# Optimization experiments

Hardware: AMD Instinct MI355X
Metric: run time of the kernel (lower is better)

## Reference

```python
import jax, jax.numpy as jnp
import numpy as np

EPS = 1e-5  # BatchNorm eps (torch default); BN is in training mode with gamma=1, beta=0 (init values)


def bn(x, axes):
    m = jnp.mean(x, axis=axes, keepdims=True)
    v = jnp.var(x, axis=axes, keepdims=True)
    return (x - m) * jax.lax.rsqrt(v + EPS)


def knn_idx(xyz, k):
    # brute-force squared-distance matrix [B,N,N], k smallest
    d = jnp.sum((xyz[:, :, None, :] - xyz[:, None, :, :]) ** 2, axis=-1)
    _, idx = jax.lax.top_k(-d, k)
    return idx  # [B,N,k]


def gather(x, idx):
    # x: [B,N,C], idx: [B,N,k] -> [B,N,k,C]
    return jax.vmap(lambda a, i: a[i])(x, idx)


def lse(xyz, features, idx, w):
    nbr_xyz = gather(xyz, idx)                       # [B,N,k,3]
    rel = nbr_xyz - xyz[:, :, None, :]
    dist = jnp.sqrt(jnp.maximum(jnp.sum(rel ** 2, -1, keepdims=True), 1e-12))
    nbr_f = gather(features, idx)                    # [B,N,k,C]
    enc = jnp.concatenate([rel, dist, nbr_f], -1)    # [B,N,k,C+4]
    return jax.nn.relu(bn(jnp.einsum('bnkc,oc->bnko', enc, w), (0, 1, 2)))


def att_pool(x, sw1, sw2, sb2, mw):
    # x: [B,N,k,C]
    h = jax.nn.relu(bn(jnp.einsum('bnkc,oc->bnko', x, sw1), (0, 1, 2)))
    scores = jax.nn.softmax(jnp.einsum('bnkc,oc->bnko', h, sw2) + sb2, axis=2)  # softmax over k
    feat = jnp.sum(x * scores, axis=2)               # [B,N,C]
    return jax.nn.relu(bn(jnp.einsum('bnc,oc->bno', feat, mw), (0, 1)))


def drb(x, w1, w2):
    # in_channels == out_channels -> identity shortcut
    h = jax.nn.relu(bn(jnp.einsum('bnc,oc->bno', x, w1), (0, 1)))
    h = bn(jnp.einsum('bnc,oc->bno', h, w2), (0, 1))
    return jax.nn.relu(h + x)


def setup_inputs() -> dict:
    key = jax.random.key(0)
    B, N, C, K, OUT = 4, 8192, 32, 16, 128
    H = OUT // 2  # 64
    ks = jax.random.split(key, 16)
    s = 0.05
    return {
        'xyz': jax.random.normal(ks[0], (B, N, 3), jnp.float32),
        'features': jax.random.normal(ks[1], (B, N, C), jnp.float32),
        'w_lse1': jax.random.normal(ks[2], (H, C + 4), jnp.float32) * s,
        'w_lse2': jax.random.normal(ks[3], (H, C + 4), jnp.float32) * s,
        'ap1_sw1': jax.random.normal(ks[4], (H, H), jnp.float32) * s,
        'ap1_sw2': jax.random.normal(ks[5], (1, H), jnp.float32) * s,
        'ap1_sb2': jax.random.normal(ks[6], (1,), jnp.float32) * s,
        'ap1_mw': jax.random.normal(ks[7], (H, H), jnp.float32) * s,
        'ap2_sw1': jax.random.normal(ks[8], (H, H), jnp.float32) * s,
        'ap2_sw2': jax.random.normal(ks[9], (1, H), jnp.float32) * s,
        'ap2_sb2': jax.random.normal(ks[10], (1,), jnp.float32) * s,
        'ap2_mw': jax.random.normal(ks[11], (H, H), jnp.float32) * s,
        'drb_w1': jax.random.normal(ks[12], (OUT, OUT), jnp.float32) * s,
        'drb_w2': jax.random.normal(ks[13], (OUT, OUT), jnp.float32) * s,
    }


def reference(xyz, features, w_lse1, w_lse2, ap1_sw1, ap1_sw2, ap1_sb2, ap1_mw,
              ap2_sw1, ap2_sw2, ap2_sb2, ap2_mw, drb_w1, drb_w2):
    K = 16
    idx = knn_idx(xyz, K)  # original calls knn twice on same xyz -> identical indices
    f1 = att_pool(lse(xyz, features, idx, w_lse1), ap1_sw1, ap1_sw2, ap1_sb2, ap1_mw)
    f2 = att_pool(lse(xyz, features, idx, w_lse2), ap2_sw1, ap2_sw2, ap2_sb2, ap2_mw)
    agg = jnp.concatenate([f1, f2], axis=-1)  # [B,N,128]
    return drb(agg, drb_w1, drb_w2)           # [B,N,128]
```

## Files before the change

kernel.cpp:

```cpp
#include <hip/hip_runtime.h>
#include <hip/hip_bf16.h>
#include <hip/hip_fp16.h>
#include <float.h>
#include <math.h>

#define DEVFN __device__ __forceinline__

DEVFN void wavefence() { __builtin_amdgcn_wave_barrier(); }

using half8 = __attribute__((ext_vector_type(8))) _Float16;
using f32x4 = __attribute__((ext_vector_type(4))) float;

namespace {
constexpr int Bq = 4, Nq = 8192, Cq = 32, Kq = 16;
constexpr int PTS = Bq * Nq;
constexpr int CH = 16;
constexpr int CAND = Nq / CH;
constexpr double ROWS = 524288.0;

constexpr int DS_Y = 0, DS_Z = 256, DS_G = 512, DS_H1 = 768, DS_H2 = 1024;

constexpr size_t OFF_KD   = 0;
constexpr size_t OFF_KJ   = (size_t)32 << 20;
constexpr size_t OFF_X0   = 0;
constexpr size_t OFF_X1   = (size_t)64 << 20;
constexpr size_t OFF_H1   = 0;
constexpr size_t OFF_H2   = (size_t)16 << 20;
constexpr size_t OFF_GRAW = (size_t)192 << 20;
constexpr size_t OFF_AGG  = (size_t)208 << 20;
constexpr size_t OFF_IDX  = (size_t)224 << 20;
constexpr size_t OFF_DST  = (size_t)226 << 20;
constexpr size_t OFF_MST  = ((size_t)226 << 20) + 10240;
constexpr size_t OFF_BNP  = ((size_t)226 << 20) + 16384;
constexpr size_t WS_NEED  = ((size_t)226 << 20) + 32768;
constexpr size_t FB_GRAW  = (size_t)64 << 20;
constexpr size_t FB_AGG   = (size_t)80 << 20;
constexpr size_t FB_H1    = (size_t)96 << 20;
constexpr size_t FB_H2    = (size_t)112 << 20;
constexpr size_t FB_IDX   = (size_t)128 << 20;
constexpr size_t FB_DST   = (size_t)130 << 20;
constexpr size_t FB_MST   = ((size_t)130 << 20) + 10240;
constexpr size_t FB_BNP   = ((size_t)130 << 20) + 16384;
}

DEVFN void ce_asc(float& a, float& b) {
  const float lo = fminf(a, b), hi = fmaxf(a, b);
  a = lo; b = hi;
}

DEVFN void topk16_update(float* __restrict__ L, float* __restrict__ d) {
#pragma unroll
  for (int k = 2; k <= 16; k <<= 1) {
#pragma unroll
    for (int j = k >> 1; j > 0; j >>= 1) {
#pragma unroll
      for (int i = 0; i < 16; ++i) {
        const int l = i ^ j;
        if (l > i) {
          if ((i & k) == 0) {
            const float lo = fminf(d[i], d[l]), hi = fmaxf(d[i], d[l]);
            d[i] = lo; d[l] = hi;
          } else {
            const float lo = fminf(d[i], d[l]), hi = fmaxf(d[i], d[l]);
            d[i] = hi; d[l] = lo;
          }
        }
      }
    }
  }
#pragma unroll
  for (int i = 0; i < 16; ++i) L[i] = fminf(L[i], d[15 - i]);
#pragma unroll
  for (int j = 8; j > 0; j >>= 1) {
#pragma unroll
    for (int i = 0; i < 16; ++i) {
      const int l = i ^ j;
      if (l > i) ce_asc(L[i], L[l]);
    }
  }
}

DEVFN float distf(const float4 c, const float qx, const float qy, const float qz) {
  const float dx = qx - c.x, dy = qy - c.y, dz = qz - c.z;
  return __fadd_rn(__fadd_rn(__fmul_rn(dx, dx), __fmul_rn(dy, dy)), __fmul_rn(dz, dz));
}

__global__ __launch_bounds__(256, 4) void knn_chunk_kernel(const float* __restrict__ xyz,
                                                           float* __restrict__ pd,
                                                           int* __restrict__ pj) {
  const int b = blockIdx.z;
  const int ch = blockIdx.y;
  const int n = blockIdx.x * 256 + threadIdx.x;
  __shared__ __align__(16) float4 tile[CAND];
  const float* xb = xyz + (size_t)b * Nq * 3;
  for (int t = threadIdx.x; t < CAND; t += 256) {
    const int j = ch * CAND + t;
    tile[t] = make_float4(xb[j * 3], xb[j * 3 + 1], xb[j * 3 + 2], 0.f);
  }
  __syncthreads();
  const float qx = xb[n * 3], qy = xb[n * 3 + 1], qz = xb[n * 3 + 2];
  float L[16];
#pragma unroll
  for (int i = 0; i < 16; ++i) L[i] = FLT_MAX;
  for (int t = 0; t < CAND; t += 16) {
    float d[16];
#pragma unroll
    for (int u = 0; u < 16; ++u) d[u] = distf(tile[t + u], qx, qy, qz);
    topk16_update(L, d);
  }
  const float kth = L[15];
  const size_t base = (((size_t)b * Nq + n) * CH + ch) * Kq;
  int cnt = 0, tfirst = -1;
  for (int t = 0; t < CAND; ++t) {
    const float d = distf(tile[t], qx, qy, qz);
    if (d < kth) { pd[base + cnt] = d; pj[base + cnt] = ch * CAND + t; ++cnt; }
    tfirst = (d == kth && tfirst < 0) ? t : tfirst;
  }
  if (cnt == 15) {
    pd[base + 15] = kth; pj[base + 15] = ch * CAND + tfirst; cnt = 16;
  }
  if (__any(cnt < 16)) {
    for (int t = 0; t < CAND; ++t) {
      const float d = distf(tile[t], qx, qy, qz);
      if (d == kth && cnt < 16) { pd[base + cnt] = d; pj[base + cnt] = ch * CAND + t; ++cnt; }
    }
  }
}

__global__ __launch_bounds__(256, 4) void knn_merge_kernel(const float* __restrict__ pd,
                                                           const int* __restrict__ pj,
                                                           int* __restrict__ idxo) {
  const int q = blockIdx.x * 256 + threadIdx.x;
  const float* dp = pd + (size_t)q * CH * Kq;
  const int* jp = pj + (size_t)q * CH * Kq;
  float L[16];
#pragma unroll
  for (int i = 0; i < 16; ++i) L[i] = FLT_MAX;
  for (int t = 0; t < CH * Kq; t += 16) {
    float d[16];
#pragma unroll
    for (int u = 0; u < 16; u += 4) {
      const float4 v = *(const float4*)(dp + t + u);
      d[u] = v.x; d[u + 1] = v.y; d[u + 2] = v.z; d[u + 3] = v.w;
    }
    topk16_update(L, d);
  }
  const float kth = L[15];
  int* op = idxo + (size_t)q * Kq;
  int cnt = 0;
  for (int t = 0; t < CH * Kq; ++t) {
    const float d = dp[t];
    if (d < kth) { op[cnt] = jp[t]; ++cnt; }
  }
  for (int t = 0; t < CH * Kq; ++t) {
    const float d = dp[t];
    if (d == kth && cnt < 16) { op[cnt] = jp[t]; ++cnt; }
  }
}

struct PF { float4 f0, f1; float nx, ny, nz; };

DEVFN PF issue_feat(const float* __restrict__ features, const float* __restrict__ xyz,
                    int p, int j, int sub) {
  const int b = p >> 13;
  const float* fr = features + ((size_t)b * Nq + j) * Cq;
  const float* xb = xyz + ((size_t)b * Nq + j) * 3;
  PF r;
  r.f0 = *(const float4*)(fr + sub * 8);
  r.f1 = *(const float4*)(fr + sub * 8 + 4);
  r.nx = xb[0]; r.ny = xb[1]; r.nz = xb[2];
  return r;
}

DEVFN int issue_idx(const int* __restrict__ idx, int p, int lane) {
  return idx[(size_t)p * Kq + (lane >> 2)];
}

DEVFN float3 issue_query(const float* __restrict__ xyz, int p) {
  const float* q = xyz + (size_t)p * 3;
  return make_float3(q[0], q[1], q[2]);
}

DEVFN void commit_enc(__half* __restrict__ enc, int lane, const PF& pf,
                      float qx, float qy, float qz) {
  const int k = lane >> 2, sub = lane & 3;
  __half* er = enc + k * 40;
  union { float4 f; __half2 h[4]; } u;
  u.h[0] = __floats2half2_rn(pf.f0.x, pf.f0.y);
  u.h[1] = __floats2half2_rn(pf.f0.z, pf.f0.w);
  u.h[2] = __floats2half2_rn(pf.f1.x, pf.f1.y);
  u.h[3] = __floats2half2_rn(pf.f1.z, pf.f1.w);
  *(float4*)(er + sub * 8) = u.f;
  if (sub == 0) {
    const float rx = pf.nx - qx, ry = pf.ny - qy, rz = pf.nz - qz;
    const float ss = rx * rx + ry * ry + rz * rz;
    const float dd = sqrtf(fmaxf(ss, 1e-12f));
    __half2* rd = (__half2*)(er + 32);
    rd[0] = __floats2half2_rn(rx, ry);
    rd[1] = __floats2half2_rn(rz, dd);
  }
}

DEVFN void commit_enc128(__half* __restrict__ enc, int lane, const PF& pf,
                         float qx, float qy, float qz) {
  const int k = lane >> 2, sub = lane & 3;
  char* base = (char*)enc + k * 128;
  union { float4 f; __half2 h[4]; } u;
  u.h[0] = __floats2half2_rn(pf.f0.x, pf.f0.y);
  u.h[1] = __floats2half2_rn(pf.f0.z, pf.f0.w);
  u.h[2] = __floats2half2_rn(pf.f1.x, pf.f1.y);
  u.h[3] = __floats2half2_rn(pf.f1.z, pf.f1.w);
  *(float4*)(base + ((sub ^ (k & 7)) * 16)) = u.f;
  if (sub == 0) {
    const float rx = pf.nx - qx, ry = pf.ny - qy, rz = pf.nz - qz;
    const float ss = rx * rx + ry * ry + rz * rz;
    const float dd = sqrtf(fmaxf(ss, 1e-12f));
    __half2* aux = (__half2*)(base + ((4 ^ (k & 7)) * 16));
    aux[0] = __floats2half2_rn(rx, ry);
    aux[1] = __floats2half2_rn(rz, dd);
  }
}

DEVFN void zero_enc_pad(__half* __restrict__ enc, int lane) {
  if (lane < 16) {
    const __half2 z2 = __floats2half2_rn(0.f, 0.f);
    __half2* pz = (__half2*)(enc + lane * 40 + 36);
    pz[0] = z2; pz[1] = z2;
  }
}

DEVFN float dot40h(const __half* __restrict__ er, const __half2* __restrict__ wh2) {
  float a0 = 0.f, a1 = 0.f, a2 = 0.f, a3 = 0.f;
#pragma unroll
  for (int r = 0; r < 5; ++r) {
    union { float4 f; __half2 h[4]; } u;
    u.f = *(const float4*)(er + r * 8);
#pragma unroll
    for (int q = 0; q < 4; ++q) {
      const __half2 xv = u.h[q];
      const __half2 wv = wh2[r * 4 + q];
      if (q & 1) {
        a2 += __low2float(xv) * __low2float(wv);
        a3 += __high2float(xv) * __high2float(wv);
      } else {
        a0 += __low2float(xv) * __low2float(wv);
        a1 += __high2float(xv) * __high2float(wv);
      }
    }
  }
  return (a0 + a1) + (a2 + a3);
}

DEVFN float dot64x(const __half* __restrict__ xr, const __half2* __restrict__ sh2) {
  float a0 = 0.f, a1 = 0.f, a2 = 0.f, a3 = 0.f;
#pragma unroll
  for (int r = 0; r < 8; ++r) {
    union { float4 f; __half2 h[4]; } u;
    u.f = *(const float4*)(xr + r * 8);
#pragma unroll
    for (int q = 0; q < 4; ++q) {
      const __half2 xv = u.h[q];
      const __half2 wv = sh2[r * 4 + q];
      if (q & 1) {
        a2 += __low2float(xv) * __low2float(wv);
        a3 += __high2float(xv) * __high2float(wv);
      } else {
        a0 += __low2float(xv) * __low2float(wv);
        a1 += __high2float(xv) * __high2float(wv);
      }
    }
  }
  return (a0 + a1) + (a2 + a3);
}

DEVFN void load_w40(const float* __restrict__ Wrow, __half2* wh2) {
#pragma unroll
  for (int c = 0; c < 16; ++c)
    wh2[c] = __floats2half2_rn(Wrow[4 + 2 * c], Wrow[5 + 2 * c]);
  wh2[16] = __floats2half2_rn(Wrow[0], Wrow[1]);
  wh2[17] = __floats2half2_rn(Wrow[2], Wrow[3]);
  wh2[18] = __floats2half2_rn(0.f, 0.f);
  wh2[19] = wh2[18];
}

DEVFN void load_b1(const float* __restrict__ W, int lane, half8* b1) {
  const int o16 = lane & 15, q = lane >> 4;
#pragma unroll
  for (int t = 0; t < 4; ++t) {
    const int o = t * 16 + o16;
#pragma unroll
    for (int ks = 0; ks < 2; ++ks) {
      half8 v;
#pragma unroll
      for (int j = 0; j < 8; ++j) {
        const int s = ks * 32 + q * 8 + j;
        float wv = 0.f;
        if (s < 36) { const int orig = (s < 32) ? (s + 4) : (s - 32); wv = W[o * 36 + orig]; }
        v[j] = (_Float16)wv;
      }
      b1[t * 2 + ks] = v;
    }
  }
}

DEVFN void load_b2(const float* __restrict__ S1, int lane, half8* b2) {
  const int o16 = lane & 15, q = lane >> 4;
#pragma unroll
  for (int t = 0; t < 4; ++t) {
    const int o = t * 16 + o16;
#pragma unroll
    for (int ks = 0; ks < 2; ++ks) {
      half8 v;
#pragma unroll
      for (int j = 0; j < 8; ++j) {
        const int c = ks * 32 + q * 8 + j;
        v[j] = (_Float16)S1[o * 64 + c];
      }
      b2[t * 2 + ks] = v;
    }
  }
}

#define GATHER_PROLOGUE                                                      \
  int p = wid;                                                               \
  int jc = issue_idx(idx, p, lane);                                          \
  PF cur = issue_feat(features, xyz, p, jc, lane & 3);                       \
  float3 qc = issue_query(xyz, p);                                           \
  int pn0 = p + nw; if (pn0 >= PTS) pn0 = p;                                 \
  int jn = issue_idx(idx, pn0, lane);                                        \
  float3 qn = issue_query(xyz, pn0);                                         \
  for (; p < PTS; p += nw) {                                                 \
    int pn = p + nw; if (pn >= PTS) pn = p;                                  \
    int pn2 = pn + nw; if (pn2 >= PTS) pn2 = pn;                             \
    PF nxt = issue_feat(features, xyz, pn, jn, lane & 3);                    \
    const int jn2 = issue_idx(idx, pn2, lane);                               \
    const float3 q2 = issue_query(xyz, pn2);                                 \
    commit_enc(enc, lane, cur, qc.x, qc.y, qc.z);                            \
    wavefence();

#define GATHER_PROLOGUE_M                                                    \
  int p = wid;                                                               \
  int jc = issue_idx(idx, p, lane);                                          \
  PF cur = issue_feat(features, xyz, p, jc, lane & 3);                       \
  float3 qc = issue_query(xyz, p);                                           \
  int pn0 = p + nw; if (pn0 >= PTS) pn0 = p;                                 \
  int jn = issue_idx(idx, pn0, lane);                                        \
  float3 qn = issue_query(xyz, pn0);                                         \
  for (; p < PTS; p += nw) {                                                 \
    int pn = p + nw; if (pn >= PTS) pn = p;                                  \
    int pn2 = pn + nw; if (pn2 >= PTS) pn2 = pn;                             \
    PF nxt = issue_feat(features, xyz, pn, jn, lane & 3);                    \
    const int jn2 = issue_idx(idx, pn2, lane);                               \
    const float3 q2 = issue_query(xyz, pn2);                                 \
    commit_enc128(enc, lane, cur, qc.x, qc.y, qc.z);                         \
    wavefence();

#define GATHER_EPILOGUE                                                      \
    wavefence();                                                             \
    cur = nxt; qc = qn; qn = q2; jn = jn2;                                   \
  }

__global__ __launch_bounds__(256) void encM_kernel(const float* __restrict__ xyz,
                                                   const float* __restrict__ features,
                                                   const int* __restrict__ idx,
                                                   float* __restrict__ mstat) {
  __shared__ __align__(16) __half encS[4][16 * 40];
  __shared__ float mred[4][36 * 37];
  const int lane = threadIdx.x & 63, wv = threadIdx.x >> 6;
  __half* enc = encS[wv];
  zero_enc_pad(enc, lane);
  wavefence();
  const int li = (lane < 36) ? lane : 0;
  float macc[36];
#pragma unroll
  for (int i = 0; i < 36; ++i) macc[i] = 0.f;
  float vacc = 0.f;
  const int wid = blockIdx.x * 4 + wv, nw = gridDim.x * 4;
  GATHER_PROLOGUE
#pragma unroll
    for (int k = 0; k < 16; ++k) {
      const __half* er = enc + k * 40;
      const float ei = __half2float(er[li]);
      vacc += ei;
#pragma unroll
      for (int r = 0; r < 5; ++r) {
        union { float4 f; __half2 h[4]; } u;
        u.f = *(const float4*)(er + r * 8);
#pragma unroll
        for (int q = 0; q < 4; ++q) {
          const int s = r * 8 + 2 * q;
          if (s < 36)     macc[s]     += ei * __low2float(u.h[q]);
          if (s + 1 < 36) macc[s + 1] += ei * __high2float(u.h[q]);
        }
      }
    }
  GATHER_EPILOGUE
  if (lane < 36) {
#pragma unroll
    for (int j = 0; j < 36; ++j) mred[wv][lane * 37 + j] = macc[j];
    mred[wv][lane * 37 + 36] = vacc;
  }
  __syncthreads();
  for (int t = threadIdx.x; t < 36 * 37; t += 256) {
    const float s = mred[0][t] + mred[1][t] + mred[2][t] + mred[3][t];
    atomicAdd(&mstat[t], s);
  }
}

__global__ void y_finalize_kernel(const float* __restrict__ mstat,
                                  const float* __restrict__ wl1,
                                  const float* __restrict__ wl2,
                                  float* __restrict__ bnp) {
  const int t = threadIdx.x;
  const int br = t >> 6, o = t & 63;
  const float* W = br ? wl2 : wl1;
  double wrow[36];
  for (int s = 0; s < 36; ++s) {
    const int orig = (s < 32) ? (s + 4) : (s - 32);
    wrow[s] = (double)W[o * 36 + orig];
  }
  double mean = 0.0, ey2 = 0.0;
  for (int i = 0; i < 36; ++i) {
    mean += wrow[i] * (double)mstat[i * 37 + 36];
    double rowacc = 0.0;
    for (int j = 0; j < 36; ++j) rowacc += wrow[j] * (double)mstat[i * 37 + j];
    ey2 += wrow[i] * rowacc;
  }
  const double invR = 1.0 / ROWS;
  mean *= invR; ey2 *= invR;
  const double var = ey2 - mean * mean;
  bnp[DS_Y + br * 64 + o] = (float)mean;
  bnp[DS_Y + 128 + br * 64 + o] = (float)(1.0 / sqrt(var + 1e-5));
}

__global__ void bn_finalize_kernel(const double* __restrict__ dstat, float* __restrict__ bnp,
                                   int base, double invc) {
  const int t = threadIdx.x;
  const double m = dstat[base + t] * invc;
  const double v = dstat[base + 128 + t] * invc - m * m;
  bnp[base + t] = (float)m;
  bnp[base + 128 + t] = (float)(1.0 / sqrt(v + 1e-5));
}

__global__ __launch_bounds__(256)
void passA2_mat_kernel(const float* __restrict__ xyz,
                       const float* __restrict__ features,
                       const int* __restrict__ idx,
                       const float* __restrict__ wl1,
                       const float* __restrict__ wl2,
                       const float* __restrict__ bnp,
                       __half* __restrict__ x0buf,
                       __half* __restrict__ x1buf) {
  __shared__ __align__(16) __half encS[4][16 * 64];
  __shared__ __align__(16) __half xS[4][16 * 64];
  const int lane = threadIdx.x & 63, wv = threadIdx.x >> 6;
  __half* enc = encS[wv];
  __half* xL = xS[wv];
  {
    const float4 z4 = {0.f, 0.f, 0.f, 0.f};
    ((float4*)enc)[lane] = z4;
    ((float4*)enc)[lane + 64] = z4;
  }
  wavefence();
  half8 b1a[8], b1b[8];
  load_b1(wl1, lane, b1a);
  load_b1(wl2, lane, b1b);
  const int r16 = lane & 15, q4 = lane >> 4;
  float ym0[4], ys0[4], ym1[4], ys1[4];
#pragma unroll
  for (int t = 0; t < 4; ++t) {
    ym0[t] = bnp[DS_Y + t * 16 + r16];
    ys0[t] = bnp[DS_Y + 128 + t * 16 + r16];
    ym1[t] = bnp[DS_Y + 64 + t * 16 + r16];
    ys1[t] = bnp[DS_Y + 128 + 64 + t * 16 + r16];
  }
  const int wid = blockIdx.x * 4 + wv, nw = gridDim.x * 4;
  GATHER_PROLOGUE_M
    const char* encb = (const char*)enc + r16 * 128;
    const half8 a0 = *(const half8*)(encb + (((q4)     ^ (r16 & 7)) * 16));
    const half8 a1 = *(const half8*)(encb + (((4 + q4) ^ (r16 & 7)) * 16));
    {
      f32x4 yt[4];
#pragma unroll
      for (int t = 0; t < 4; ++t) {
        f32x4 acc = {0.f, 0.f, 0.f, 0.f};
        acc = __builtin_amdgcn_mfma_f32_16x16x32_f16(a0, b1a[t * 2], acc, 0, 0, 0);
        acc = __builtin_amdgcn_mfma_f32_16x16x32_f16(a1, b1a[t * 2 + 1], acc, 0, 0, 0);
        yt[t] = acc;
      }
#pragma unroll
      for (int t = 0; t < 4; ++t) {
        const int col = t * 16 + r16;
        const int chk = col >> 3;
#pragma unroll
        for (int rr = 0; rr < 4; ++rr) {
          const int row = q4 * 4 + rr;
          float xv = (yt[t][rr] - ym0[t]) * ys0[t];
          xv = xv > 0.f ? xv : 0.f;
          *(_Float16*)((char*)xL + row * 128 + ((chk ^ (row & 7)) * 16) + (col & 7) * 2) =
              (_Float16)xv;
        }
      }
      wavefence();
#pragma unroll
      for (int it = 0; it < 2; ++it) {
        const int chunk = it * 64 + lane;
        const int row = chunk >> 3, c8 = chunk & 7;
        const float4 xv4 = *(const float4*)((const char*)xL + row * 128 + ((c8 ^ (row & 7)) * 16));
        *(float4*)((char*)x0buf + (size_t)p * 2048 + chunk * 16) = xv4;
      }
      wavefence();
    }
    {
      f32x4 yt[4];
#pragma unroll
      for (int t = 0; t < 4; ++t) {
        f32x4 acc = {0.f, 0.f, 0.f, 0.f};
        acc = __builtin_amdgcn_mfma_f32_16x16x32_f16(a0, b1b[t * 2], acc, 0, 0, 0);
        acc = __builtin_amdgcn_mfma_f32_16x16x32_f16(a1, b1b[t * 2 + 1], acc, 0, 0, 0);
        yt[t] = acc;
      }
#pragma unroll
      for (int t = 0; t < 4; ++t) {
        const int col = t * 16 + r16;
        const int chk = col >> 3;
#pragma unroll
        for (int rr = 0; rr < 4; ++rr) {
          const int row = q4 * 4 + rr;
          float xv = (yt[t][rr] - ym1[t]) * ys1[t];
          xv = xv > 0.f ? xv : 0.f;
          *(_Float16*)((char*)xL + row * 128 + ((chk ^ (row & 7)) * 16) + (col & 7) * 2) =
              (_Float16)xv;
        }
      }
      wavefence();
#pragma unroll
      for (int it = 0; it < 2; ++it) {
        const int chunk = it * 64 + lane;
        const int row = chunk >> 3, c8 = chunk & 7;
        const float4 xv4 = *(const float4*)((const char*)xL + row * 128 + ((c8 ^ (row & 7)) * 16));
        *(float4*)((char*)x1buf + (size_t)p * 2048 + chunk * 16) = xv4;
      }
    }
  GATHER_EPILOGUE
}

__global__ __launch_bounds__(256)
void zstat_kernel(const __half* __restrict__ x0, const __half* __restrict__ x1,
                  const float* __restrict__ s1a, const float* __restrict__ s1b,
                  double* __restrict__ dstat) {
  const int lane = threadIdx.x & 63, wv = threadIdx.x >> 6;
  half8 b2a[8], b2b[8];
  load_b2(s1a, lane, b2a);
  load_b2(s1b, lane, b2b);
  const int r16 = lane & 15, q4 = lane >> 4;
  float sa1[4] = {0.f, 0.f, 0.f, 0.f}, sa2[4] = {0.f, 0.f, 0.f, 0.f};
  float sb1[4] = {0.f, 0.f, 0.f, 0.f}, sb2s[4] = {0.f, 0.f, 0.f, 0.f};
  const int wid = blockIdx.x * 4 + wv, nw = gridDim.x * 4;
  for (int p = wid; p < PTS; p += nw) {
    const size_t abase = (size_t)p * 1024 + r16 * 64 + q4 * 8;
    const half8 xa0 = *(const half8*)(x0 + abase);
    const half8 xa1 = *(const half8*)(x0 + abase + 32);
    const half8 xb0 = *(const half8*)(x1 + abase);
    const half8 xb1 = *(const half8*)(x1 + abase + 32);
#pragma unroll
    for (int t = 0; t < 4; ++t) {
      f32x4 acc = {0.f, 0.f, 0.f, 0.f};
      acc = __builtin_amdgcn_mfma_f32_16x16x32_f16(xa0, b2a[t * 2], acc, 0, 0, 0);
      acc = __builtin_amdgcn_mfma_f32_16x16x32_f16(xa1, b2a[t * 2 + 1], acc, 0, 0, 0);
#pragma unroll
      for (int rr = 0; rr < 4; ++rr) { const float zv = acc[rr]; sa1[t] += zv; sa2[t] += zv * zv; }
      f32x4 acc2 = {0.f, 0.f, 0.f, 0.f};
      acc2 = __builtin_amdgcn_mfma_f32_16x16x32_f16(xb0, b2b[t * 2], acc2, 0, 0, 0);
      acc2 = __builtin_amdgcn_mfma_f32_16x16x32_f16(xb1, b2b[t * 2 + 1], acc2, 0, 0, 0);
#pragma unroll
      for (int rr = 0; rr < 4; ++rr) { const float zv = acc2[rr]; sb1[t] += zv; sb2s[t] += zv * zv; }
    }
  }
#pragma unroll
  for (int t = 0; t < 4; ++t) {
    sa1[t] += __shfl_xor(sa1[t], 16, 64);  sa1[t] += __shfl_xor(sa1[t], 32, 64);
    sa2[t] += __shfl_xor(sa2[t], 16, 64);  sa2[t] += __shfl_xor(sa2[t], 32, 64);
    sb1[t] += __shfl_xor(sb1[t], 16, 64);  sb1[t] += __shfl_xor(sb1[t], 32, 64);
    sb2s[t] += __shfl_xor(sb2s[t], 16, 64); sb2s[t] += __shfl_xor(sb2s[t], 32, 64);
  }
  if (lane < 16) {
#pragma unroll
    for (int t = 0; t < 4; ++t) {
      atomicAdd(&dstat[DS_Z + t * 16 + lane], (double)sa1[t]);
      atomicAdd(&dstat[DS_Z + 128 + t * 16 + lane], (double)sa2[t]);
      atomicAdd(&dstat[DS_Z + 64 + t * 16 + lane], (double)sb1[t]);
      atomicAdd(&dstat[DS_Z + 128 + 64 + t * 16 + lane], (double)sb2s[t]);
    }
  }
}

__global__ __launch_bounds__(256)
void passB2_mat_kernel(const __half* __restrict__ xbuf,
                       const float* __restrict__ S1,
                       const float* __restrict__ s2,
                       const float* __restrict__ sb,
                       const float* __restrict__ mw,
                       const float* __restrict__ bnp,
                       double* __restrict__ dstat,
                       float* __restrict__ graw,
                       int br) {
  __shared__ __align__(16) __half2 mwl2[64 * 34];
  __shared__ __align__(16) float featL[4][64];
  __shared__ __align__(16) float zS[4][16 * 64];
  for (int t = threadIdx.x; t < 64 * 32; t += 256) {
    const int r = t >> 5, c2 = t & 31;
    mwl2[r * 34 + c2] = __floats2half2_rn(mw[r * 64 + c2 * 2], mw[r * 64 + c2 * 2 + 1]);
  }
  __syncthreads();
  const int lane = threadIdx.x & 63, wv = threadIdx.x >> 6;
  const int r16 = lane & 15, q4 = lane >> 4;
  half8 b2[8];
  load_b2(S1, lane, b2);
  const __half2* mrow = mwl2 + lane * 34;
  const float zm = bnp[DS_Z + br * 64 + lane];
  const float zsc = bnp[DS_Z + 128 + br * 64 + lane];
  const float sw2r = s2[lane];
  const float sb2v = sb[0];
  float gs1 = 0.f, gs2 = 0.f;
  float* zw = &zS[wv][0];
  const int wid = blockIdx.x * 4 + wv, nw = gridDim.x * 4;
  for (int p = wid; p < PTS; p += nw) {
    const size_t abase = (size_t)p * 1024 + r16 * 64 + q4 * 8;
    const half8 xa0 = *(const half8*)(xbuf + abase);
    const half8 xa1 = *(const half8*)(xbuf + abase + 32);
#pragma unroll
    for (int t = 0; t < 4; ++t) {
      f32x4 acc = {0.f, 0.f, 0.f, 0.f};
      acc = __builtin_amdgcn_mfma_f32_16x16x32_f16(xa0, b2[t * 2], acc, 0, 0, 0);
      acc = __builtin_amdgcn_mfma_f32_16x16x32_f16(xa1, b2[t * 2 + 1], acc, 0, 0, 0);
#pragma unroll
      for (int rr = 0; rr < 4; ++rr)
        zw[(q4 * 4 + rr) * 64 + t * 16 + r16] = acc[rr];
    }
    wavefence();
    const __half* xr = xbuf + (size_t)p * 1024 + lane;
    const float* zr = zw + lane;
    float xv[16], pl[16];
#pragma unroll
    for (int k = 0; k < 16; ++k) {
      xv[k] = __half2float(xr[k * 64]);
      float h = (zr[k * 64] - zm) * zsc;
      h = h > 0.f ? h : 0.f;
      pl[k] = h * sw2r;
    }
#pragma unroll
    for (int off = 1; off < 64; off <<= 1) {
#pragma unroll
      for (int k = 0; k < 16; ++k) pl[k] += __shfl_xor(pl[k], off, 64);
    }
    float mx = -FLT_MAX;
#pragma unroll
    for (int k = 0; k < 16; ++k) { pl[k] += sb2v; mx = fmaxf(mx, pl[k]); }
    float se = 0.f;
#pragma unroll
    for (int k = 0; k < 16; ++k) { pl[k] = expf(pl[k] - mx); se += pl[k]; }
    const float inv = 1.f / se;
    float f = 0.f;
#pragma unroll
    for (int k = 0; k < 16; ++k) f += xv[k] * (pl[k] * inv);
    featL[wv][lane] = f;
    wavefence();
    const float* featW = &featL[wv][0];
    float g0 = 0.f, g1 = 0.f, g2 = 0.f, g3 = 0.f;
#pragma unroll
    for (int c8 = 0; c8 < 8; ++c8) {
      const float4 fa = *(const float4*)(featW + c8 * 8);
      const float4 fb = *(const float4*)(featW + c8 * 8 + 4);
      const __half2 m0 = mrow[c8 * 4 + 0];
      const __half2 m1 = mrow[c8 * 4 + 1];
      const __half2 m2 = mrow[c8 * 4 + 2];
      const __half2 m3 = mrow[c8 * 4 + 3];
      g0 += fa.x * __low2float(m0); g1 += fa.y * __high2float(m0);
      g2 += fa.z * __low2float(m1); g3 += fa.w * __high2float(m1);
      g0 += fb.x * __low2float(m2); g1 += fb.y * __high2float(m2);
      g2 += fb.z * __low2float(m3); g3 += fb.w * __high2float(m3);
    }
    const float g = (g0 + g1) + (g2 + g3);
    graw[((size_t)br * PTS + p) * 64 + lane] = g;
    gs1 += g; gs2 += g * g;
    wavefence();
  }
  atomicAdd(&dstat[DS_G + br * 64 + lane], (double)gs1);
  atomicAdd(&dstat[DS_G + 128 + br * 64 + lane], (double)gs2);
}

__global__ __launch_bounds__(256)
void passA_kernel(const float* __restrict__ xyz,
                  const float* __restrict__ features,
                  const int* __restrict__ idx,
                  const float* __restrict__ wl1,
                  const float* __restrict__ wl2,
                  const float* __restrict__ s1a,
                  const float* __restrict__ s1b,
                  const float* __restrict__ bnp,
                  double* __restrict__ dstat) {
  const int br = blockIdx.y;
  const float* W = br ? wl2 : wl1;
  const float* S1 = br ? s1b : s1a;
  __shared__ __align__(16) __half encS[4][16 * 40];
  __shared__ __align__(16) __half xS[4][16 * 64];
  const int lane = threadIdx.x & 63, wv = threadIdx.x >> 6;
  __half* enc = encS[wv];
  __half* xL = xS[wv];
  zero_enc_pad(enc, lane);
  wavefence();
  __half2 wh2[20];
  load_w40(W + lane * 36, wh2);
  __half2 sh2[32];
#pragma unroll
  for (int c = 0; c < 32; ++c)
    sh2[c] = __floats2half2_rn(S1[lane * 64 + 2 * c], S1[lane * 64 + 2 * c + 1]);
  const float ym = bnp[DS_Y + br * 64 + lane];
  const float ys = bnp[DS_Y + 128 + br * 64 + lane];
  float zs1 = 0.f, zs2 = 0.f;
  const int wid = blockIdx.x * 4 + wv, nw = gridDim.x * 4;
  GATHER_PROLOGUE
#pragma unroll
    for (int k = 0; k < 16; ++k) {
      float xv = (dot40h(enc + k * 40, wh2) - ym) * ys;
      xv = xv > 0.f ? xv : 0.f;
      xL[k * 64 + lane] = __float2half(xv);
    }
    wavefence();
#pragma unroll
    for (int k = 0; k < 16; ++k) {
      const float acc = dot64x(xL + k * 64, sh2);
      zs1 += acc; zs2 += acc * acc;
    }
  GATHER_EPILOGUE
  atomicAdd(&dstat[DS_Z + br * 64 + lane], (double)zs1);
  atomicAdd(&dstat[DS_Z + 128 + br * 64 + lane], (double)zs2);
}

__global__ __launch_bounds__(256)
void passB_kernel(const float* __restrict__ xyz,
                  const float* __restrict__ features,
                  const int* __restrict__ idx,
                  const float* __restrict__ wl1,
                  const float* __restrict__ wl2,
                  const float* __restrict__ s1a,
                  const float* __restrict__ s1b,
                  const float* __restrict__ s2a,
                  const float* __restrict__ s2b,
                  const float* __restrict__ sba,
                  const float* __restrict__ sbb,
                  const float* __restrict__ mwa,
                  const float* __restrict__ mwb,
                  const float* __restrict__ bnp,
                  double* __restrict__ dstat,
                  float* __restrict__ graw) {
  const int br = blockIdx.y;
  const float* W = br ? wl2 : wl1;
  const float* S1 = br ? s1b : s1a;
  const float* S2 = br ? s2b : s2a;
  const float* SB = br ? sbb : sba;
  const float* MW = br ? mwb : mwa;
  __shared__ __align__(16) __half2 mwl2[64 * 34];
  __shared__ __align__(16) __half encS[4][16 * 40];
  __shared__ __align__(16) __half xS[4][16 * 64];
  __shared__ __align__(16) float featL[4][64];
  for (int t = threadIdx.x; t < 64 * 32; t += 256) {
    const int r = t >> 5, c2 = t & 31;
    mwl2[r * 34 + c2] = __floats2half2_rn(MW[r * 64 + c2 * 2], MW[r * 64 + c2 * 2 + 1]);
  }
  __syncthreads();
  const int lane = threadIdx.x & 63, wv = threadIdx.x >> 6;
  __half* enc = encS[wv];
  __half* xL = xS[wv];
  zero_enc_pad(enc, lane);
  wavefence();
  const __half2* mrow = mwl2 + lane * 34;
  __half2 wh2[20];
  load_w40(W + lane * 36, wh2);
  __half2 sh2[32];
#pragma unroll
  for (int c = 0; c < 32; ++c)
    sh2[c] = __floats2half2_rn(S1[lane * 64 + 2 * c], S1[lane * 64 + 2 * c + 1]);
  const float ym = bnp[DS_Y + br * 64 + lane];
  const float ys = bnp[DS_Y + 128 + br * 64 + lane];
  const float zm = bnp[DS_Z + br * 64 + lane];
  const float zs = bnp[DS_Z + 128 + br * 64 + lane];
  const float sw2r = S2[lane];
  const float sb2v = SB[0];
  float gs1 = 0.f, gs2 = 0.f;
  const int wid = blockIdx.x * 4 + wv, nw = gridDim.x * 4;
  GATHER_PROLOGUE
#pragma unroll
    for (int k = 0; k < 16; ++k) {
      float xv = (dot40h(enc + k * 40, wh2) - ym) * ys;
      xv = xv > 0.f ? xv : 0.f;
      xL[k * 64 + lane] = __float2half(xv);
    }
    wavefence();
    float pl[16];
#pragma unroll
    for (int k = 0; k < 16; ++k) {
      float h = (dot64x(xL + k * 64, sh2) - zm) * zs;
      h = h > 0.f ? h : 0.f;
      pl[k] = h * sw2r;
    }
#pragma unroll
    for (int off = 1; off < 64; off <<= 1) {
#pragma unroll
      for (int k = 0; k < 16; ++k) pl[k] += __shfl_xor(pl[k], off, 64);
    }
    float mx = -FLT_MAX;
#pragma unroll
    for (int k = 0; k < 16; ++k) { pl[k] += sb2v; mx = fmaxf(mx, pl[k]); }
    float se = 0.f;
#pragma unroll
    for (int k = 0; k < 16; ++k) { pl[k] = expf(pl[k] - mx); se += pl[k]; }
    const float inv = 1.f / se;
    float f = 0.f;
#pragma unroll
    for (int k = 0; k < 16; ++k) f += __half2float(xL[k * 64 + lane]) * (pl[k] * inv);
    featL[wv][lane] = f;
    wavefence();
    const float* featW = &featL[wv][0];
    float g0 = 0.f, g1 = 0.f, g2 = 0.f, g3 = 0.f;
#pragma unroll
    for (int c8 = 0; c8 < 8; ++c8) {
      const float4 fa = *(const float4*)(featW + c8 * 8);
      const float4 fb = *(const float4*)(featW + c8 * 8 + 4);
      const __half2 m0 = mrow[c8 * 4 + 0];
      const __half2 m1 = mrow[c8 * 4 + 1];
      const __half2 m2 = mrow[c8 * 4 + 2];
      const __half2 m3 = mrow[c8 * 4 + 3];
      g0 += fa.x * __low2float(m0); g1 += fa.y * __high2float(m0);
      g2 += fa.z * __low2float(m1); g3 += fa.w * __high2float(m1);
      g0 += fb.x * __low2float(m2); g1 += fb.y * __high2float(m2);
      g2 += fb.z * __low2float(m3); g3 += fb.w * __high2float(m3);
    }
    const float g = (g0 + g1) + (g2 + g3);
    graw[((size_t)br * PTS + p) * 64 + lane] = g;
    gs1 += g; gs2 += g * g;
  GATHER_EPILOGUE
  atomicAdd(&dstat[DS_G + br * 64 + lane], (double)gs1);
  atomicAdd(&dstat[DS_G + 128 + br * 64 + lane], (double)gs2);
}

__global__ __launch_bounds__(256) void drb_mm_kernel(const float* __restrict__ in,
                                                     const float* __restrict__ wmat,
                                                     const float* __restrict__ bnp,
                                                     double* __restrict__ dstat,
                                                     float* __restrict__ aggout,
                                                     float* __restrict__ rowout,
                                                     int bpIn, int dsOut, int mode) {
  __shared__ __align__(16) float wlds[128 * 129];
  __shared__ __align__(16) float rowS[4][128];
  for (int t = threadIdx.x; t < 128 * 128; t += 256) wlds[(t >> 7) * 129 + (t & 127)] = wmat[t];
  __syncthreads();
  const int lane = threadIdx.x & 63, wv = threadIdx.x >> 6;
  const float m0 = bnp[bpIn + lane], s0 = bnp[bpIn + 128 + lane];
  const float m1 = bnp[bpIn + 64 + lane], s1 = bnp[bpIn + 128 + 64 + lane];
  float a1s0 = 0.f, a1s1 = 0.f, a2s0 = 0.f, a2s1 = 0.f;
  const int wid = blockIdx.x * 4 + wv, nw = gridDim.x * 4;
  for (int p = wid; p < PTS; p += nw) {
    float v0, v1;
    if (mode == 0) {
      v0 = in[(size_t)p * 64 + lane];
      v1 = in[(size_t)PTS * 64 + (size_t)p * 64 + lane];
    } else {
      v0 = in[(size_t)p * 128 + lane];
      v1 = in[(size_t)p * 128 + 64 + lane];
    }
    v0 = (v0 - m0) * s0; v0 = v0 > 0.f ? v0 : 0.f;
    v1 = (v1 - m1) * s1; v1 = v1 > 0.f ? v1 : 0.f;
    rowS[wv][lane] = v0;
    rowS[wv][64 + lane] = v1;
    if (aggout) {
      aggout[(size_t)p * 128 + lane] = v0;
      aggout[(size_t)p * 128 + 64 + lane] = v1;
    }
    wavefence();
#pragma unroll
    for (int h = 0; h < 2; ++h) {
      const int o = h * 64 + lane;
      float b0 = 0.f, b1 = 0.f, b2 = 0.f, b3 = 0.f;
#pragma unroll
      for (int c4 = 0; c4 < 32; ++c4) {
        const float4 rv = *(const float4*)(&rowS[wv][c4 * 4]);
        b0 += rv.x * wlds[o * 129 + c4 * 4 + 0];
        b1 += rv.y * wlds[o * 129 + c4 * 4 + 1];
        b2 += rv.z * wlds[o * 129 + c4 * 4 + 2];
        b3 += rv.w * wlds[o * 129 + c4 * 4 + 3];
      }
      const float acc = (b0 + b1) + (b2 + b3);
      rowout[(size_t)p * 128 + o] = acc;
      if (h == 0) { a1s0 += acc; a2s0 += acc * acc; }
      else        { a1s1 += acc; a2s1 += acc * acc; }
    }
    wavefence();
  }
  atomicAdd(&dstat[dsOut + lane], (double)a1s0);
  atomicAdd(&dstat[dsOut + 64 + lane], (double)a1s1);
  atomicAdd(&dstat[dsOut + 128 + lane], (double)a2s0);
  atomicAdd(&dstat[dsOut + 128 + 64 + lane], (double)a2s1);
}

__global__ __launch_bounds__(256) void final_kernel(const float* __restrict__ h2,
                                                    const float* __restrict__ agg,
                                                    const float* __restrict__ bnp,
                                                    float* __restrict__ out) {
  const size_t e = (size_t)blockIdx.x * 256 + threadIdx.x;
  const int ch = (int)(e & 127);
  const float m = bnp[DS_H2 + ch], s = bnp[DS_H2 + 128 + ch];
  float v = (h2[e] - m) * s + agg[e];
  out[e] = v > 0.f ? v : 0.f;
}

extern "C" void kernel_launch(void* const* d_in, const int* in_sizes, int n_in,
                              void* d_out, int out_size, void* d_ws, size_t ws_size,
                              hipStream_t stream) {
  (void)in_sizes; (void)n_in; (void)out_size;
  const float* xyz      = (const float*)d_in[0];
  const float* features = (const float*)d_in[1];
  const float* w_lse1   = (const float*)d_in[2];
  const float* w_lse2   = (const float*)d_in[3];
  const float* ap1_sw1  = (const float*)d_in[4];
  const float* ap1_sw2  = (const float*)d_in[5];
  const float* ap1_sb2  = (const float*)d_in[6];
  const float* ap1_mw   = (const float*)d_in[7];
  const float* ap2_sw1  = (const float*)d_in[8];
  const float* ap2_sw2  = (const float*)d_in[9];
  const float* ap2_sb2  = (const float*)d_in[10];
  const float* ap2_mw   = (const float*)d_in[11];
  const float* drb_w1   = (const float*)d_in[12];
  const float* drb_w2   = (const float*)d_in[13];

  char* ws = (char*)d_ws;
  const bool mat = (ws_size >= WS_NEED);

  float*  knn_d = (float*)(ws + OFF_KD);
  int*    knn_j = (int*)(ws + OFF_KJ);
  int*    idx   = (int*)(ws + (mat ? OFF_IDX : FB_IDX));
  double* dstat = (double*)(ws + (mat ? OFF_DST : FB_DST));
  float*  mstat = (float*)(ws + (mat ? OFF_MST : FB_MST));
  float*  bnp   = (float*)(ws + (mat ? OFF_BNP : FB_BNP));
  float*  graw  = (float*)(ws + (mat ? OFF_GRAW : FB_GRAW));
  float*  agg   = (float*)(ws + (mat ? OFF_AGG : FB_AGG));
  float*  h1    = (float*)(ws + (mat ? OFF_H1 : FB_H1));
  float*  h2    = (float*)(ws + (mat ? OFF_H2 : FB_H2));
  float*  out   = (float*)d_out;

  (void)hipMemsetAsync(dstat, 0, 1280 * sizeof(double) + 36 * 37 * sizeof(float), stream);

  knn_chunk_kernel<<<dim3(Nq / 256, CH, Bq), 256, 0, stream>>>(xyz, knn_d, knn_j);
  knn_merge_kernel<<<dim3(PTS / 256), 256, 0, stream>>>(knn_d, knn_j, idx);

  encM_kernel<<<dim3(1280), 256, 0, stream>>>(xyz, features, idx, mstat);
  y_finalize_kernel<<<1, 128, 0, stream>>>(mstat, w_lse1, w_lse2, bnp);

  if (mat) {
    __half* x0 = (__half*)(ws + OFF_X0);
    __half* x1 = (__half*)(ws + OFF_X1);
    passA2_mat_kernel<<<dim3(1280), 256, 0, stream>>>(xyz, features, idx, w_lse1, w_lse2,
                                                      bnp, x0, x1);
    zstat_kernel<<<dim3(1024), 256, 0, stream>>>(x0, x1, ap1_sw1, ap2_sw1, dstat);
    bn_finalize_kernel<<<1, 128, 0, stream>>>(dstat, bnp, DS_Z, 1.0 / ROWS);
    passB2_mat_kernel<<<dim3(1024), 256, 0, stream>>>(x0, ap1_sw1, ap1_sw2, ap1_sb2,
                                                      ap1_mw, bnp, dstat, graw, 0);
    passB2_mat_kernel<<<dim3(1024), 256, 0, stream>>>(x1, ap2_sw1, ap2_sw2, ap2_sb2,
                                                      ap2_mw, bnp, dstat, graw, 1);
  } else {
    passA_kernel<<<dim3(640, 2), 256, 0, stream>>>(xyz, features, idx, w_lse1, w_lse2,
                                                   ap1_sw1, ap2_sw1, bnp, dstat);
    bn_finalize_kernel<<<1, 128, 0, stream>>>(dstat, bnp, DS_Z, 1.0 / ROWS);
    passB_kernel<<<dim3(512, 2), 256, 0, stream>>>(xyz, features, idx, w_lse1, w_lse2,
                                                   ap1_sw1, ap2_sw1, ap1_sw2, ap2_sw2,
                                                   ap1_sb2, ap2_sb2, ap1_mw, ap2_mw,
                                                   bnp, dstat, graw);
  }
  bn_finalize_kernel<<<1, 128, 0, stream>>>(dstat, bnp, DS_G, 1.0 / PTS);

  drb_mm_kernel<<<dim3(512), 256, 0, stream>>>(graw, drb_w1, bnp, dstat, agg, h1,
                                               DS_G, DS_H1, 0);
  bn_finalize_kernel<<<1, 128, 0, stream>>>(dstat, bnp, DS_H1, 1.0 / PTS);

  drb_mm_kernel<<<dim3(512), 256, 0, stream>>>(h1, drb_w2, bnp, dstat, nullptr, h2,
                                               DS_H1, DS_H2, 1);
  bn_finalize_kernel<<<1, 128, 0, stream>>>(dstat, bnp, DS_H2, 1.0 / PTS);

  final_kernel<<<dim3(PTS * 128 / 256), 256, 0, stream>>>(h2, agg, bnp, out);
}
```

Measured before the change: 1.259 ms.

## Materialize fp16 neighbor encodings in encM and stream them in passA2

The moment-statistics kernel now writes each point's 16x40 fp16 neighbor encoding to a workspace buffer. The second pass reads that buffer with contiguous loads instead of redoing the random neighbor gathers from xyz/features and rebuilding the swizzled LDS encoding. This trades repeated scattered gathers and the extra LDS staging for about 40 MB of extra global writes and reads. The grid size of the second pass also changes.

```diff
diff --git a/kernel.cpp b/kernel.cpp
--- a/kernel.cpp
+++ b/kernel.cpp
@@ -24,6 +24,7 @@
 constexpr size_t OFF_KJ   = (size_t)32 << 20;
 constexpr size_t OFF_X0   = 0;
 constexpr size_t OFF_X1   = (size_t)64 << 20;
+constexpr size_t OFF_ENC  = (size_t)128 << 20;
 constexpr size_t OFF_H1   = 0;
 constexpr size_t OFF_H2   = (size_t)16 << 20;
 constexpr size_t OFF_GRAW = (size_t)192 << 20;
@@ -201,26 +202,6 @@
   }
 }
 
-DEVFN void commit_enc128(__half* __restrict__ enc, int lane, const PF& pf,
-                         float qx, float qy, float qz) {
-  const int k = lane >> 2, sub = lane & 3;
-  char* base = (char*)enc + k * 128;
-  union { float4 f; __half2 h[4]; } u;
-  u.h[0] = __floats2half2_rn(pf.f0.x, pf.f0.y);
-  u.h[1] = __floats2half2_rn(pf.f0.z, pf.f0.w);
-  u.h[2] = __floats2half2_rn(pf.f1.x, pf.f1.y);
-  u.h[3] = __floats2half2_rn(pf.f1.z, pf.f1.w);
-  *(float4*)(base + ((sub ^ (k & 7)) * 16)) = u.f;
-  if (sub == 0) {
-    const float rx = pf.nx - qx, ry = pf.ny - qy, rz = pf.nz - qz;
-    const float ss = rx * rx + ry * ry + rz * rz;
-    const float dd = sqrtf(fmaxf(ss, 1e-12f));
-    __half2* aux = (__half2*)(base + ((4 ^ (k & 7)) * 16));
-    aux[0] = __floats2half2_rn(rx, ry);
-    aux[1] = __floats2half2_rn(rz, dd);
-  }
-}
-
 DEVFN void zero_enc_pad(__half* __restrict__ enc, int lane) {
   if (lane < 16) {
     const __half2 z2 = __floats2half2_rn(0.f, 0.f);
@@ -338,23 +319,6 @@
     commit_enc(enc, lane, cur, qc.x, qc.y, qc.z);                            \
     wavefence();
 
-#define GATHER_PROLOGUE_M                                                    \
-  int p = wid;                                                               \
-  int jc = issue_idx(idx, p, lane);                                          \
-  PF cur = issue_feat(features, xyz, p, jc, lane & 3);                       \
-  float3 qc = issue_query(xyz, p);                                           \
-  int pn0 = p + nw; if (pn0 >= PTS) pn0 = p;                                 \
-  int jn = issue_idx(idx, pn0, lane);                                        \
-  float3 qn = issue_query(xyz, pn0);                                         \
-  for (; p < PTS; p += nw) {                                                 \
-    int pn = p + nw; if (pn >= PTS) pn = p;                                  \
-    int pn2 = pn + nw; if (pn2 >= PTS) pn2 = pn;                             \
-    PF nxt = issue_feat(features, xyz, pn, jn, lane & 3);                    \
-    const int jn2 = issue_idx(idx, pn2, lane);                               \
-    const float3 q2 = issue_query(xyz, pn2);                                 \
-    commit_enc128(enc, lane, cur, qc.x, qc.y, qc.z);                         \
-    wavefence();
-
 #define GATHER_EPILOGUE                                                      \
     wavefence();                                                             \
     cur = nxt; qc = qn; qn = q2; jn = jn2;                                   \
@@ -363,7 +327,8 @@
 __global__ __launch_bounds__(256) void encM_kernel(const float* __restrict__ xyz,
                                                    const float* __restrict__ features,
                                                    const int* __restrict__ idx,
-                                                   float* __restrict__ mstat) {
+                                                   float* __restrict__ mstat,
+                                                   __half* __restrict__ encb) {
   __shared__ __align__(16) __half encS[4][16 * 40];
   __shared__ float mred[4][36 * 37];
   const int lane = threadIdx.x & 63, wv = threadIdx.x >> 6;
@@ -391,6 +356,16 @@
           const int s = r * 8 + 2 * q;
           if (s < 36)     macc[s]     += ei * __low2float(u.h[q]);
           if (s + 1 < 36) macc[s + 1] += ei * __high2float(u.h[q]);
+        }
+      }
+    }
+    if (encb) {
+#pragma unroll
+      for (int it = 0; it < 2; ++it) {
+        const int c = it * 64 + lane;
+        if (c < 80) {
+          const float4 v = *(const float4*)((const char*)enc + c * 16);
+          *(float4*)((char*)encb + (size_t)p * 1280 + c * 16) = v;
         }
       }
     }
@@ -443,25 +418,15 @@
 }
 
 __global__ __launch_bounds__(256)
-void passA2_mat_kernel(const float* __restrict__ xyz,
-                       const float* __restrict__ features,
-                       const int* __restrict__ idx,
-                       const float* __restrict__ wl1,
-                       const float* __restrict__ wl2,
-                       const float* __restrict__ bnp,
-                       __half* __restrict__ x0buf,
-                       __half* __restrict__ x1buf) {
-  __shared__ __align__(16) __half encS[4][16 * 64];
+void passA2s_kernel(const __half* __restrict__ encbuf,
+                    const float* __restrict__ wl1,
+                    const float* __restrict__ wl2,
+                    const float* __restrict__ bnp,
+                    __half* __restrict__ x0buf,
+                    __half* __restrict__ x1buf) {
   __shared__ __align__(16) __half xS[4][16 * 64];
   const int lane = threadIdx.x & 63, wv = threadIdx.x >> 6;
-  __half* enc = encS[wv];
   __half* xL = xS[wv];
-  {
-    const float4 z4 = {0.f, 0.f, 0.f, 0.f};
-    ((float4*)enc)[lane] = z4;
-    ((float4*)enc)[lane + 64] = z4;
-  }
-  wavefence();
   half8 b1a[8], b1b[8];
   load_b1(wl1, lane, b1a);
   load_b1(wl2, lane, b1b);
@@ -475,10 +440,13 @@
     ys1[t] = bnp[DS_Y + 128 + 64 + t * 16 + r16];
   }
   const int wid = blockIdx.x * 4 + wv, nw = gridDim.x * 4;
-  GATHER_PROLOGUE_M
-    const char* encb = (const char*)enc + r16 * 128;
-    const half8 a0 = *(const half8*)(encb + (((q4)     ^ (r16 & 7)) * 16));
-    const half8 a1 = *(const half8*)(encb + (((4 + q4) ^ (r16 & 7)) * 16));
+  for (int p = wid; p < PTS; p += nw) {
+    const size_t eb = (size_t)p * 640 + r16 * 40 + q4 * 8;
+    const half8 a0 = *(const half8*)(encbuf + eb);
+    half8 a1;
+#pragma unroll
+    for (int j = 0; j < 8; ++j) a1[j] = (_Float16)0.f;
+    if (q4 == 0) a1 = *(const half8*)(encbuf + eb + 32);
     {
       f32x4 yt[4];
 #pragma unroll
@@ -541,8 +509,9 @@
         const float4 xv4 = *(const float4*)((const char*)xL + row * 128 + ((c8 ^ (row & 7)) * 16));
         *(float4*)((char*)x1buf + (size_t)p * 2048 + chunk * 16) = xv4;
       }
-    }
-  GATHER_EPILOGUE
+      wavefence();
+    }
+  }
 }
 
 __global__ __launch_bounds__(256)
@@ -954,14 +923,14 @@
   knn_chunk_kernel<<<dim3(Nq / 256, CH, Bq), 256, 0, stream>>>(xyz, knn_d, knn_j);
   knn_merge_kernel<<<dim3(PTS / 256), 256, 0, stream>>>(knn_d, knn_j, idx);
 
-  encM_kernel<<<dim3(1280), 256, 0, stream>>>(xyz, features, idx, mstat);
+  __half* encb = mat ? (__half*)(ws + OFF_ENC) : nullptr;
+  encM_kernel<<<dim3(1280), 256, 0, stream>>>(xyz, features, idx, mstat, encb);
   y_finalize_kernel<<<1, 128, 0, stream>>>(mstat, w_lse1, w_lse2, bnp);
 
   if (mat) {
     __half* x0 = (__half*)(ws + OFF_X0);
     __half* x1 = (__half*)(ws + OFF_X1);
-    passA2_mat_kernel<<<dim3(1280), 256, 0, stream>>>(xyz, features, idx, w_lse1, w_lse2,
-                                                      bnp, x0, x1);
+    passA2s_kernel<<<dim3(1024), 256, 0, stream>>>(encb, w_lse1, w_lse2, bnp, x0, x1);
     zstat_kernel<<<dim3(1024), 256, 0, stream>>>(x0, x1, ap1_sw1, ap2_sw1, dstat);
     bn_finalize_kernel<<<1, 128, 0, stream>>>(dstat, bnp, DS_Z, 1.0 / ROWS);
     passB2_mat_kernel<<<dim3(1024), 256, 0, stream>>>(x0, ap1_sw1, ap1_sw2, ap1_sb2,
```

After: 1.276 ms. Within noise of the previous version (+1.3%).
